# Optimization experiments

Measured on AMD Instinct MI355X. Metric: run time of the kernel, lower is better.

## Reference

```python
import jax, jax.numpy as jnp
import numpy as np

B, C, H, W = 2, 128, 256, 510
WF = W // 2 + 1  # 256 == H; required so var [B,C,H,1] broadcasts against scores [B,C,WF,WF]


def setup_inputs() -> dict:
    key = jax.random.key(0)
    ks = jax.random.split(key, 8)
    f = lambda k, s: jax.random.normal(k, s, dtype=jnp.float32)
    return {
        "g": f(ks[0], (B, C, H, W)),
        "x": f(ks[1], (B, C, H, W)),
        "wg_conv": f(ks[2], (C, C)) * 0.05,   # 1x1 conv inside Gate_signle GlobalFilter
        "bg_conv": jnp.zeros((C,), jnp.float32),
        "wx_conv": f(ks[3], (C, C)) * 0.05,   # 1x1 conv inside Wieghts_signle GlobalFilter
        "bx_conv": jnp.zeros((C,), jnp.float32),
        "filt_g": f(ks[4], (C, H, WF, 2)) * 0.02,  # learned complex freq filter (re, im)
        "filt_x": f(ks[5], (C, H, WF, 2)) * 0.02,
        "ln_gamma": jnp.ones((C,), jnp.float32),
        "ln_beta": jnp.zeros((C,), jnp.float32),
    }


def _global_filter_freq(x, w, b, filt):
    # 1x1 conv (channel mix) then GFNet-style complex frequency filtering.
    y = jnp.einsum('bchw,oc->bohw', x, w) + b[None, :, None, None]
    f = jnp.fft.rfft2(y, axes=(2, 3), norm='ortho')            # [B,C,H,WF] complex64
    wc = (filt[..., 0] + 1j * filt[..., 1]).astype(f.dtype)    # [C,H,WF]
    return f * wc[None]


def _sigmoid_complex(z):
    return jax.nn.sigmoid(z.real) + 1j * jax.nn.sigmoid(z.imag)


def reference(g, x, wg_conv, bg_conv, wx_conv, bx_conv, filt_g, filt_x, ln_gamma, ln_beta):
    g1_feq = _global_filter_freq(g, wg_conv, bg_conv, filt_g)  # [B,C,H,WF]
    x1_feq = _global_filter_freq(x, wx_conv, bx_conv, filt_x)  # [B,C,H,WF]
    # Varaince: detached, biased, over last dim, keepdims (real-valued for complex input)
    norm_frwq = jax.lax.stop_gradient(jnp.var(g1_feq, axis=-1, keepdims=True))  # [B,C,H,1]
    # frequency-domain attention: transpose(2,3) @ -> [B,C,WF,WF]
    scores = jnp.matmul(jnp.swapaxes(g1_feq, 2, 3), x1_feq) / jnp.sqrt(2.0 * jnp.pi * norm_frwq)
    atten = _sigmoid_complex(scores)
    inverse_atten = jnp.fft.irfft2(atten, s=(H, W), axes=(2, 3), norm='ortho')  # [B,C,H,W]
    r = inverse_atten + x
    # LayerNorm(F_int): channels-first LN over channel dim
    mu = jnp.mean(r, axis=1, keepdims=True)
    s2 = jnp.mean((r - mu) ** 2, axis=1, keepdims=True)
    return ln_gamma[None, :, None, None] * (r - mu) / jnp.sqrt(s2 + 1e-6) + ln_beta[None, :, None, None]
```

## Files before the change

kernel.cpp:

```cpp
#include <hip/hip_runtime.h>

typedef unsigned short u16t;
typedef __attribute__((ext_vector_type(4))) u16t us4;
typedef __attribute__((ext_vector_type(8))) u16t us8;
typedef __attribute__((ext_vector_type(8))) short mf8;
typedef __attribute__((ext_vector_type(4))) float f4;

#define BB 2
#define CCH 128
#define HHH 256
#define WWW 510
#define WFQ 256
#define HWP 130560
#define NROW 65536
#define UPL 16777216L
#define YPAD 512

__device__ __forceinline__ float u2f(u16t v){ return __uint_as_float(((unsigned)v)<<16); }
__device__ __forceinline__ u16t  f2u(float f){
  unsigned u = __float_as_uint(f);
  return (u16t)((u + 0x7fffu + ((u>>16)&1u)) >> 16);
}
__device__ __forceinline__ float ldin(const void* p, long i, int f32){
  return f32 ? ((const float*)p)[i] : u2f(((const u16t*)p)[i]);
}
__device__ __forceinline__ float sigm(float z){ return 1.f/(1.f+__expf(-z)); }
__device__ __forceinline__ f4 z4(){ f4 v; v[0]=0.f;v[1]=0.f;v[2]=0.f;v[3]=0.f; return v; }

__device__ __forceinline__ f4 MF(us8 a, us8 b, f4 c){
  return __builtin_amdgcn_mfma_f32_16x16x32_bf16((mf8)a, (mf8)b, c, 0, 0, 0);
}

__device__ __forceinline__ us8 frg(const u16t* tile, int row, int g){
  return *(const us8*)(tile + (row<<5) + (((g)^(row&3))<<3));
}
__device__ __forceinline__ void stg(u16t* __restrict__ tile, const u16t* __restrict__ src,
                                    long base, int pitch, int nu, int t){
  #pragma unroll
  for(int i=0;i<nu;i++){
    int e = t + 256*i;
    int row = e>>2, slot = e&3;
    us8 v = *(const us8*)(src + base + (long)row*pitch + (slot<<3));
    *(us8*)(tile + (row<<5) + ((slot^(row&3))<<3)) = v;
  }
}

__global__ void k_detect(const void* __restrict__ g, int* __restrict__ flag){
  __shared__ int cnt[256];
  int t = threadIdx.x;
  const u16t* pb = (const u16t*)g;
  int c = 0;
  for(int i=0;i<16;i++){
    int idx = t*16 + i;
    float v = u2f(pb[2*idx]);
    unsigned bits = __float_as_uint(v);
    int ex = (bits>>23)&0xff;
    if(ex >= 117 && ex <= 137) c++;
  }
  cnt[t]=c; __syncthreads();
  for(int s=128;s>0;s>>=1){ if(t<s) cnt[t]+=cnt[t+s]; __syncthreads(); }
  if(t==0) *flag = (cnt[0] < 2048) ? 1 : 0;
}

__device__ __forceinline__ void hl(u16t* ph, u16t* pl, long i, float v){
  u16t h = f2u(v); ph[i] = h;
  pl[i] = f2u(v - u2f(h));
}
__global__ void k_tables2(u16t* twch, u16t* twcl, u16t* twsh, u16t* twsl,
                          u16t* thch, u16t* thcl, u16t* thsh, u16t* thsl,
                          u16t* tich, u16t* ticl, u16t* tish, u16t* tisl){
  long idx = (long)blockIdx.x*256 + threadIdx.x;
  const float s510 = rsqrtf(510.0f);
  const float TP = 6.283185307179586f;
  {
    int n = (int)(idx>>9), w = (int)(idx&511);
    float c = 0.f, s = 0.f;
    if(w < 510){
      float ang = (TP/510.0f)*(float)((w*n)%510);
      c =  cosf(ang)*s510;
      s = -sinf(ang)*s510;
    }
    hl(twch, twcl, idx, c);
    hl(twsh, twsl, idx, s);
  }
  if(idx < 65536){
    int m = (int)(idx>>8), k = (int)(idx&255);
    float ang = (TP/256.0f)*(float)((m*k)&255);
    hl(thch, thcl, idx, cosf(ang)*0.0625f);
    hl(thsh, thsl, idx, sinf(ang)*0.0625f);
  }
  {
    int w = (int)(idx>>8), k = (int)(idx&255);
    float c = 0.f, s = 0.f;
    if(w < 510){
      float ck = (k==0 || k==255) ? 1.0f : 2.0f;
      float ang = (TP/510.0f)*(float)((k*w)%510);
      c =  ck*cosf(ang)*s510;
      s = -ck*sinf(ang)*s510;
    }
    hl(tich, ticl, idx, c);
    hl(tish, tisl, idx, s);
  }
}

__global__ void k_zpad(u16t* __restrict__ Y){
  int i = blockIdx.x*256 + threadIdx.x;
  long row = i>>1;
  Y[row*YPAD + 510 + (i&1)] = 0;
}

__global__ __launch_bounds__(256) void k_conv2(const void* __restrict__ in,
    const void* __restrict__ wmat, const void* __restrict__ bias,
    const int* __restrict__ flagp, u16t* __restrict__ Y){
  __shared__ __align__(16) u16t Aw[4096], Bh[4096], Bl[4096];
  __shared__ float sb[128];
  int f32 = *flagp;
  int t=threadIdx.x, l=t&63, wid=t>>6, wr=wid>>1, wc=wid&1;
  int hw0 = blockIdx.x*128, b = blockIdx.y;
  if(t<128) sb[t] = ldin(bias, t, f32);
  long inb = (long)b*CCH*HWP;
  f4 acc[4][4];
  #pragma unroll
  for(int i=0;i<4;i++) for(int j=0;j<4;j++) acc[i][j]=z4();
  for(int c0=0;c0<128;c0+=32){
    __syncthreads();
    #pragma unroll
    for(int i=0;i<2;i++){
      int e = t + 256*i; int row = e>>2, slot = e&3;
      u16t tmp[8];
      #pragma unroll
      for(int j=0;j<8;j++) tmp[j] = f2u(ldin(wmat, (long)row*128 + c0 + (slot<<3) + j, f32));
      *(us8*)(Aw + (row<<5) + ((slot^(row&3))<<3)) = *(us8*)tmp;
    }
    {
      int n = t&127, kb = (t>>7)*16;
      u16t th[16], tl[16];
      #pragma unroll
      for(int j=0;j<16;j++){
        float v = ldin(in, inb + (long)(c0+kb+j)*HWP + hw0 + n, f32);
        u16t h = f2u(v); th[j]=h;
        tl[j] = f2u(v - u2f(h));
      }
      int s0 = kb>>3;
      *(us8*)(Bh + (n<<5) + (((s0  )^(n&3))<<3)) = *(us8*)&th[0];
      *(us8*)(Bh + (n<<5) + (((s0+1)^(n&3))<<3)) = *(us8*)&th[8];
      *(us8*)(Bl + (n<<5) + (((s0  )^(n&3))<<3)) = *(us8*)&tl[0];
      *(us8*)(Bl + (n<<5) + (((s0+1)^(n&3))<<3)) = *(us8*)&tl[8];
    }
    __syncthreads();
    int lr=l&15, g=l>>4;
    us8 a[4];
    #pragma unroll
    for(int mm=0;mm<4;mm++) a[mm]=frg(Aw, wr*64+mm*16+lr, g);
    #pragma unroll
    for(int nn=0;nn<4;nn++){
      int rn = wc*64+nn*16+lr;
      us8 bh=frg(Bh,rn,g), bl=frg(Bl,rn,g);
      #pragma unroll
      for(int mm=0;mm<4;mm++){
        acc[mm][nn]=MF(a[mm],bh,acc[mm][nn]);
        acc[mm][nn]=MF(a[mm],bl,acc[mm][nn]);
      }
    }
  }
  int lr=l&15, g=l>>4;
  #pragma unroll
  for(int nn=0;nn<4;nn++){
    int hw = hw0 + wc*64 + nn*16 + lr;
    int h = hw/510, w = hw - h*510;
    #pragma unroll
    for(int mm=0;mm<4;mm++){
      #pragma unroll
      for(int r=0;r<4;r++){
        int o = wr*64 + mm*16 + (g<<2) + r;
        Y[((long)(b*128 + o)*256 + h)*YPAD + w] = f2u(acc[mm][nn][r] + sb[o]);
      }
    }
  }
}

__global__ __launch_bounds__(256) void k_rfft2(const u16t* __restrict__ Y,
    const u16t* __restrict__ twch, const u16t* __restrict__ twcl,
    const u16t* __restrict__ twsh, const u16t* __restrict__ twsl,
    u16t* __restrict__ Grt, u16t* __restrict__ Git){
  __shared__ __align__(16) u16t At[4096], Bch[4096], Bcl[4096], Bsh[4096], Bsl[4096];
  int t=threadIdx.x, l=t&63, wid=t>>6, wr=wid>>1, wc=wid&1;
  int m0 = blockIdx.x*128, n0 = blockIdx.y*128;
  f4 accr[4][4], acci[4][4];
  #pragma unroll
  for(int i=0;i<4;i++) for(int j=0;j<4;j++){ accr[i][j]=z4(); acci[i][j]=z4(); }
  for(int k0=0;k0<512;k0+=32){
    __syncthreads();
    stg(At,  Y,    (long)m0*YPAD + k0, YPAD, 2, t);
    stg(Bch, twch, (long)n0*512  + k0, 512,  2, t);
    stg(Bcl, twcl, (long)n0*512  + k0, 512,  2, t);
    stg(Bsh, twsh, (long)n0*512  + k0, 512,  2, t);
    stg(Bsl, twsl, (long)n0*512  + k0, 512,  2, t);
    __syncthreads();
    int lr=l&15, g=l>>4;
    us8 a[4];
    #pragma unroll
    for(int mm=0;mm<4;mm++) a[mm]=frg(At, wr*64+mm*16+lr, g);
    #pragma unroll
    for(int nn=0;nn<4;nn++){
      int rn = wc*64+nn*16+lr;
      us8 bch=frg(Bch,rn,g), bcl=frg(Bcl,rn,g), bsh=frg(Bsh,rn,g), bsl=frg(Bsl,rn,g);
      #pragma unroll
      for(int mm=0;mm<4;mm++){
        accr[mm][nn]=MF(a[mm],bch,accr[mm][nn]); accr[mm][nn]=MF(a[mm],bcl,accr[mm][nn]);
        acci[mm][nn]=MF(a[mm],bsh,acci[mm][nn]); acci[mm][nn]=MF(a[mm],bsl,acci[mm][nn]);
      }
    }
  }
  int plane = blockIdx.x>>1;
  int h0 = (blockIdx.x&1)<<7;
  int lr=l&15, g=l>>4;
  #pragma unroll
  for(int nn=0;nn<4;nn++){
    int n = n0 + wc*64 + nn*16 + lr;
    #pragma unroll
    for(int mm=0;mm<4;mm++){
      int hh = h0 + wr*64 + mm*16 + (g<<2);
      long o = (long)plane*65536 + (long)n*256 + hh;
      us4 pr, pi;
      #pragma unroll
      for(int r=0;r<4;r++){ pr[r]=f2u(accr[mm][nn][r]); pi[r]=f2u(acci[mm][nn][r]); }
      *(us4*)(Grt+o)=pr; *(us4*)(Git+o)=pi;
    }
  }
}

__global__ __launch_bounds__(256) void k_ffth2(
    const u16t* __restrict__ Br_, const u16t* __restrict__ Bi_,
    const u16t* __restrict__ ach_, const u16t* __restrict__ acl_,
    const u16t* __restrict__ ash_, const u16t* __restrict__ asl_,
    float sgn, int tr_out, const void* __restrict__ filt, const int* __restrict__ flagp,
    u16t* __restrict__ Or_, u16t* __restrict__ Oi_){
  __shared__ __align__(16) u16t Ach[2048], Acl[2048], Ash[2048], Asl[2048], Bgr[2048], Bgi[2048];
  int t=threadIdx.x, l=t&63, wid=t>>6, wr=wid>>1, wc=wid&1;
  int m0=blockIdx.x*64, n0=blockIdx.y*64, plane=blockIdx.z;
  long pbase=(long)plane*65536;
  f4 P1[2][2],P2[2][2],P3[2][2],P4[2][2];
  #pragma unroll
  for(int i=0;i<2;i++) for(int j=0;j<2;j++){ P1[i][j]=z4();P2[i][j]=z4();P3[i][j]=z4();P4[i][j]=z4(); }
  for(int k0=0;k0<256;k0+=32){
    __syncthreads();
    stg(Ach, ach_, (long)m0*256+k0, 256, 1, t);
    stg(Acl, acl_, (long)m0*256+k0, 256, 1, t);
    stg(Ash, ash_, (long)m0*256+k0, 256, 1, t);
    stg(Asl, asl_, (long)m0*256+k0, 256, 1, t);
    stg(Bgr, Br_, pbase+(long)n0*256+k0, 256, 1, t);
    stg(Bgi, Bi_, pbase+(long)n0*256+k0, 256, 1, t);
    __syncthreads();
    int lr=l&15, g=l>>4;
    us8 fch[2],fcl[2],fsh[2],fsl[2];
    #pragma unroll
    for(int mm=0;mm<2;mm++){
      int rr=wr*32+mm*16+lr;
      fch[mm]=frg(Ach,rr,g); fcl[mm]=frg(Acl,rr,g); fsh[mm]=frg(Ash,rr,g); fsl[mm]=frg(Asl,rr,g);
    }
    #pragma unroll
    for(int nn=0;nn<2;nn++){
      int rn=wc*32+nn*16+lr;
      us8 bgr=frg(Bgr,rn,g), bgi=frg(Bgi,rn,g);
      #pragma unroll
      for(int mm=0;mm<2;mm++){
        P1[mm][nn]=MF(fch[mm],bgr,P1[mm][nn]); P1[mm][nn]=MF(fcl[mm],bgr,P1[mm][nn]);
        P2[mm][nn]=MF(fsh[mm],bgi,P2[mm][nn]); P2[mm][nn]=MF(fsl[mm],bgi,P2[mm][nn]);
        P3[mm][nn]=MF(fch[mm],bgi,P3[mm][nn]); P3[mm][nn]=MF(fcl[mm],bgi,P3[mm][nn]);
        P4[mm][nn]=MF(fsh[mm],bgr,P4[mm][nn]); P4[mm][nn]=MF(fsl[mm],bgr,P4[mm][nn]);
      }
    }
  }
  int f32 = filt ? *flagp : 0;
  int lr=l&15, g=l>>4;
  int c_ch = plane & 127;
  #pragma unroll
  for(int nn=0;nn<2;nn++){
    int n = n0 + wc*32 + nn*16 + lr;
    #pragma unroll
    for(int mm=0;mm<2;mm++){
      int mb = m0 + wr*32 + mm*16 + (g<<2);
      float vr[4], vi[4];
      #pragma unroll
      for(int r=0;r<4;r++){
        vr[r] = P1[mm][nn][r] + sgn*P2[mm][nn][r];
        vi[r] = P3[mm][nn][r] - sgn*P4[mm][nn][r];
      }
      if(filt){
        #pragma unroll
        for(int r=0;r<4;r++){
          long fi = (((long)c_ch*256 + (mb+r))*256 + n)*2;
          float fwr=ldin(filt,fi,f32), fwi=ldin(filt,fi+1,f32);
          float a=vr[r], b=vi[r];
          vr[r]=a*fwr-b*fwi; vi[r]=a*fwi+b*fwr;
        }
      }
      if(tr_out){
        us4 pr, pi;
        #pragma unroll
        for(int r=0;r<4;r++){ pr[r]=f2u(vr[r]); pi[r]=f2u(vi[r]); }
        *(us4*)(Or_ + pbase + (long)n*256 + mb) = pr;
        *(us4*)(Oi_ + pbase + (long)n*256 + mb) = pi;
      } else {
        #pragma unroll
        for(int r=0;r<4;r++){
          Or_[pbase + (long)(mb+r)*256 + n] = f2u(vr[r]);
          Oi_[pbase + (long)(mb+r)*256 + n] = f2u(vi[r]);
        }
      }
    }
  }
}

__global__ __launch_bounds__(1024) void k_var2(const u16t* __restrict__ Grt,
    const u16t* __restrict__ Git, float* __restrict__ rinv){
  __shared__ float rs[1024], is_[1024], qs[1024];
  int plane = blockIdx.x, t = threadIdx.x;
  int kh = t & 255, part = t >> 8;
  long base = (long)plane*65536 + kh;
  float sr=0.f, si=0.f, s2=0.f;
  #pragma unroll 4
  for(int q=0;q<64;q++){
    long o = base + (long)(part*64+q)*256;
    float r = u2f(Grt[o]), im = u2f(Git[o]);
    sr += r; si += im; s2 += r*r + im*im;
  }
  rs[t]=sr; is_[t]=si; qs[t]=s2;
  __syncthreads();
  if(t<256){
    sr = rs[t]+rs[t+256]+rs[t+512]+rs[t+768];
    si = is_[t]+is_[t+256]+is_[t+512]+is_[t+768];
    s2 = qs[t]+qs[t+256]+qs[t+512]+qs[t+768];
    float mr = sr*(1.f/256.f), mi = si*(1.f/256.f);
    float v = s2*(1.f/256.f) - mr*mr - mi*mi;
    rinv[plane*256 + kh] = rsqrtf(6.283185307179586f * fmaxf(v, 1e-20f));
  }
}

__global__ __launch_bounds__(256) void k_scores2(
    const u16t* __restrict__ Agr_, const u16t* __restrict__ Agi_,
    const u16t* __restrict__ Bxr_, const u16t* __restrict__ Bxi_,
    const float* __restrict__ rinv, u16t* __restrict__ Sr_, u16t* __restrict__ Si_){
  __shared__ __align__(16) u16t Agr[2048], Agi[2048], Bxr[2048], Bxi[2048];
  int t=threadIdx.x, l=t&63, wid=t>>6, wr=wid>>1, wc=wid&1;
  int m0=blockIdx.x*64, n0=blockIdx.y*64, plane=blockIdx.z;
  long pbase=(long)plane*65536;
  f4 P1[2][2],P2[2][2],P3[2][2],P4[2][2];
  #pragma unroll
  for(int i=0;i<2;i++) for(int j=0;j<2;j++){ P1[i][j]=z4();P2[i][j]=z4();P3[i][j]=z4();P4[i][j]=z4(); }
  for(int k0=0;k0<256;k0+=32){
    __syncthreads();
    stg(Agr, Agr_, pbase+(long)m0*256+k0, 256, 1, t);
    stg(Agi, Agi_, pbase+(long)m0*256+k0, 256, 1, t);
    stg(Bxr, Bxr_, pbase+(long)n0*256+k0, 256, 1, t);
    stg(Bxi, Bxi_, pbase+(long)n0*256+k0, 256, 1, t);
    __syncthreads();
    int lr=l&15, g=l>>4;
    us8 agr[2], agi[2];
    #pragma unroll
    for(int mm=0;mm<2;mm++){
      int rr=wr*32+mm*16+lr;
      agr[mm]=frg(Agr,rr,g); agi[mm]=frg(Agi,rr,g);
    }
    #pragma unroll
    for(int nn=0;nn<2;nn++){
      int rn=wc*32+nn*16+lr;
      us8 bxr=frg(Bxr,rn,g), bxi=frg(Bxi,rn,g);
      #pragma unroll
      for(int mm=0;mm<2;mm++){
        P1[mm][nn]=MF(agr[mm],bxr,P1[mm][nn]);
        P2[mm][nn]=MF(agi[mm],bxi,P2[mm][nn]);
        P3[mm][nn]=MF(agr[mm],bxi,P3[mm][nn]);
        P4[mm][nn]=MF(agi[mm],bxr,P4[mm][nn]);
      }
    }
  }
  int lr=l&15, g=l>>4;
  #pragma unroll
  for(int nn=0;nn<2;nn++){
    int n = n0 + wc*32 + nn*16 + lr;
    #pragma unroll
    for(int mm=0;mm<2;mm++){
      int mb = m0 + wr*32 + mm*16 + (g<<2);
      us4 pr, pi;
      #pragma unroll
      for(int r=0;r<4;r++){
        float rv = rinv[(plane<<8) + mb + r];
        pr[r] = f2u(sigm((P1[mm][nn][r]-P2[mm][nn][r])*rv));
        pi[r] = f2u(sigm((P3[mm][nn][r]+P4[mm][nn][r])*rv));
      }
      *(us4*)(Sr_ + pbase + (long)n*256 + mb) = pr;
      *(us4*)(Si_ + pbase + (long)n*256 + mb) = pi;
    }
  }
}

__global__ __launch_bounds__(256) void k_irfft2(
    const u16t* __restrict__ Tr, const u16t* __restrict__ Ti,
    const u16t* __restrict__ tich, const u16t* __restrict__ ticl,
    const u16t* __restrict__ tish, const u16t* __restrict__ tisl,
    const void* __restrict__ xin, const int* __restrict__ flagp, float* __restrict__ R){
  __shared__ __align__(16) u16t Ar[4096], Ai[4096], Bch[4096], Bcl[4096], Bsh[4096], Bsl[4096];
  int t=threadIdx.x, l=t&63, wid=t>>6, wr=wid>>1, wc=wid&1;
  int m0=blockIdx.x*128, n0=blockIdx.y*128;
  f4 acc[4][4];
  #pragma unroll
  for(int i=0;i<4;i++) for(int j=0;j<4;j++) acc[i][j]=z4();
  for(int k0=0;k0<256;k0+=32){
    __syncthreads();
    stg(Ar,  Tr,   (long)m0*256+k0, 256, 2, t);
    stg(Ai,  Ti,   (long)m0*256+k0, 256, 2, t);
    stg(Bch, tich, (long)n0*256+k0, 256, 2, t);
    stg(Bcl, ticl, (long)n0*256+k0, 256, 2, t);
    stg(Bsh, tish, (long)n0*256+k0, 256, 2, t);
    stg(Bsl, tisl, (long)n0*256+k0, 256, 2, t);
    __syncthreads();
    int lr=l&15, g=l>>4;
    us8 ar[4], ai[4];
    #pragma unroll
    for(int mm=0;mm<4;mm++){
      int rr = wr*64+mm*16+lr;
      ar[mm]=frg(Ar,rr,g); ai[mm]=frg(Ai,rr,g);
    }
    #pragma unroll
    for(int nn=0;nn<4;nn++){
      int rn = wc*64+nn*16+lr;
      us8 bch=frg(Bch,rn,g), bcl=frg(Bcl,rn,g), bsh=frg(Bsh,rn,g), bsl=frg(Bsl,rn,g);
      #pragma unroll
      for(int mm=0;mm<4;mm++){
        acc[mm][nn]=MF(ar[mm],bch,acc[mm][nn]); acc[mm][nn]=MF(ar[mm],bcl,acc[mm][nn]);
        acc[mm][nn]=MF(ai[mm],bsh,acc[mm][nn]); acc[mm][nn]=MF(ai[mm],bsl,acc[mm][nn]);
      }
    }
  }
  int f32=*flagp;
  int lr=l&15, g=l>>4;
  #pragma unroll
  for(int nn=0;nn<4;nn++){
    int w = n0 + wc*64 + nn*16 + lr;
    if(w >= 510) continue;
    #pragma unroll
    for(int mm=0;mm<4;mm++){
      int row0 = m0 + wr*64 + mm*16 + (g<<2);
      #pragma unroll
      for(int r=0;r<4;r++){
        long o = (long)(row0+r)*510 + w;
        R[o] = acc[mm][nn][r] + ldin(xin, o, f32);
      }
    }
  }
}

__global__ __launch_bounds__(256) void k_ln(const float* __restrict__ R,
    const void* __restrict__ gamma, const void* __restrict__ beta,
    const int* __restrict__ flagp, void* __restrict__ out){
  int f32 = *flagp;
  int p = blockIdx.x*256 + threadIdx.x;
  int b = p / HWP, hw = p % HWP;
  long base = (long)b*CCH*HWP + hw;
  float sum=0.f, sq=0.f;
  for(int c=0;c<CCH;c++){
    float v = R[base + (long)c*HWP];
    sum += v; sq += v*v;
  }
  float mu = sum*(1.f/128.f);
  float var = sq*(1.f/128.f) - mu*mu;
  float inv = rsqrtf(fmaxf(var,0.f) + 1e-6f);
  for(int c=0;c<CCH;c++){
    float v = (R[base + (long)c*HWP] - mu)*inv;
    float o = ldin(gamma,c,f32)*v + ldin(beta,c,f32);
    long oi = base + (long)c*HWP;
    if(f32) ((float*)out)[oi] = o;
    else    ((u16t*)out)[oi]  = f2u(o);
  }
}

extern "C" void kernel_launch(void* const* d_in, const int* in_sizes, int n_in,
                              void* d_out, int out_size, void* d_ws, size_t ws_size,
                              hipStream_t stream) {
  const void* g   = d_in[0];
  const void* x   = d_in[1];
  const void* wg  = d_in[2];
  const void* bg  = d_in[3];
  const void* wx  = d_in[4];
  const void* bx  = d_in[5];
  const void* fg  = d_in[6];
  const void* fx  = d_in[7];
  const void* gam = d_in[8];
  const void* bet = d_in[9];

  u16t* Y  = (u16t*)d_ws;
  u16t* Bq = Y  + 33554432L;
  u16t* Cq = Bq + 33554432L;
  char* pp = (char*)d_ws + 201326592L;
  float* rinv = (float*)pp; pp += 262144L;
  u16t* twch=(u16t*)pp; pp+=262144L;  u16t* twcl=(u16t*)pp; pp+=262144L;
  u16t* twsh=(u16t*)pp; pp+=262144L;  u16t* twsl=(u16t*)pp; pp+=262144L;
  u16t* thch=(u16t*)pp; pp+=131072L;  u16t* thcl=(u16t*)pp; pp+=131072L;
  u16t* thsh=(u16t*)pp; pp+=131072L;  u16t* thsl=(u16t*)pp; pp+=131072L;
  u16t* tich=(u16t*)pp; pp+=262144L;  u16t* ticl=(u16t*)pp; pp+=262144L;
  u16t* tish=(u16t*)pp; pp+=262144L;  u16t* tisl=(u16t*)pp; pp+=262144L;
  int* flag = (int*)pp;
  float* R  = (float*)d_ws;

  k_detect <<<1,256,0,stream>>>(g, flag);
  k_tables2<<<512,256,0,stream>>>(twch,twcl,twsh,twsl,thch,thcl,thsh,thsl,tich,ticl,tish,tisl);
  k_zpad   <<<512,256,0,stream>>>(Y);

  k_conv2<<<dim3(1020,2),256,0,stream>>>(g, wg, bg, flag, Y);
  k_rfft2<<<dim3(512,2),256,0,stream>>>(Y, twch,twcl,twsh,twsl, Bq, Bq+UPL);
  k_ffth2<<<dim3(4,4,256),256,0,stream>>>(Bq, Bq+UPL, thch,thcl,thsh,thsl, 1.f, 1, fg, flag, Cq, Cq+UPL);

  k_conv2<<<dim3(1020,2),256,0,stream>>>(x, wx, bx, flag, Y);
  k_rfft2<<<dim3(512,2),256,0,stream>>>(Y, twch,twcl,twsh,twsl, Bq, Bq+UPL);
  k_ffth2<<<dim3(4,4,256),256,0,stream>>>(Bq, Bq+UPL, thch,thcl,thsh,thsl, 1.f, 1, fx, flag, Y, Y+UPL);

  k_var2<<<256,1024,0,stream>>>(Cq, Cq+UPL, rinv);

  k_scores2<<<dim3(4,4,256),256,0,stream>>>(Cq, Cq+UPL, Y, Y+UPL, rinv, Bq, Bq+UPL);

  k_ffth2<<<dim3(4,4,256),256,0,stream>>>(Bq, Bq+UPL, thch,thcl,thsh,thsl, -1.f, 0, nullptr, flag, Cq, Cq+UPL);

  k_irfft2<<<dim3(512,4),256,0,stream>>>(Cq, Cq+UPL, tich,ticl,tish,tisl, x, flag, R);

  k_ln<<<1020,256,0,stream>>>(R, gam, bet, flag, d_out);
}
```

Measured before the change: 1.554 ms.

## Register-prefetch next K tile, change LDS swizzle, drop low-part twiddles in inverse path

Each GEMM-style kernel (conv, rfft, ffth, scores, irfft) now loads the next K-slice of global data into registers while the current slice is consumed from LDS. This overlaps global latency with MFMA work. The LDS XOR swizzle changes from row&3 to (row>>1)&3 to alter the bank-conflict pattern. The inverse column FFT and irfft drop the bf16 low-part twiddle MFMAs, halving their matrix work at some accuracy cost. The cost is extra register pressure from the prefetch buffers.

```diff
diff --git a/kernel.cpp b/kernel.cpp
--- a/kernel.cpp
+++ b/kernel.cpp
@@ -31,17 +31,26 @@
   return __builtin_amdgcn_mfma_f32_16x16x32_bf16((mf8)a, (mf8)b, c, 0, 0, 0);
 }
 
+__device__ __forceinline__ int swz(int row){ return (row>>1)&3; }
+
 __device__ __forceinline__ us8 frg(const u16t* tile, int row, int g){
-  return *(const us8*)(tile + (row<<5) + (((g)^(row&3))<<3));
-}
-__device__ __forceinline__ void stg(u16t* __restrict__ tile, const u16t* __restrict__ src,
+  return *(const us8*)(tile + (row<<5) + (((g)^swz(row))<<3));
+}
+__device__ __forceinline__ void ldt(us8* v, const u16t* __restrict__ src,
                                     long base, int pitch, int nu, int t){
   #pragma unroll
   for(int i=0;i<nu;i++){
     int e = t + 256*i;
     int row = e>>2, slot = e&3;
-    us8 v = *(const us8*)(src + base + (long)row*pitch + (slot<<3));
-    *(us8*)(tile + (row<<5) + ((slot^(row&3))<<3)) = v;
+    v[i] = *(const us8*)(src + base + (long)row*pitch + (slot<<3));
+  }
+}
+__device__ __forceinline__ void stt(u16t* __restrict__ tile, const us8* v, int nu, int t){
+  #pragma unroll
+  for(int i=0;i<nu;i++){
+    int e = t + 256*i;
+    int row = e>>2, slot = e&3;
+    *(us8*)(tile + (row<<5) + ((slot^swz(row))<<3)) = v[i];
   }
 }
 
@@ -119,33 +128,43 @@
   int hw0 = blockIdx.x*128, b = blockIdx.y;
   if(t<128) sb[t] = ldin(bias, t, f32);
   long inb = (long)b*CCH*HWP;
+  int bn = t&127, bkb = (t>>7)*16, bs0 = bkb>>3;
   f4 acc[4][4];
   #pragma unroll
   for(int i=0;i<4;i++) for(int j=0;j<4;j++) acc[i][j]=z4();
+  float pa[16], pb[16];
+  #pragma unroll
+  for(int i=0;i<2;i++){ int e=t+256*i; int row=e>>2, slot=e&3;
+    #pragma unroll
+    for(int j=0;j<8;j++) pa[i*8+j] = ldin(wmat, (long)row*128 + (slot<<3) + j, f32); }
+  #pragma unroll
+  for(int j=0;j<16;j++) pb[j] = ldin(in, inb + (long)(bkb+j)*HWP + hw0 + bn, f32);
+
   for(int c0=0;c0<128;c0+=32){
     __syncthreads();
     #pragma unroll
-    for(int i=0;i<2;i++){
-      int e = t + 256*i; int row = e>>2, slot = e&3;
+    for(int i=0;i<2;i++){ int e=t+256*i; int row=e>>2, slot=e&3;
       u16t tmp[8];
       #pragma unroll
-      for(int j=0;j<8;j++) tmp[j] = f2u(ldin(wmat, (long)row*128 + c0 + (slot<<3) + j, f32));
-      *(us8*)(Aw + (row<<5) + ((slot^(row&3))<<3)) = *(us8*)tmp;
-    }
+      for(int j=0;j<8;j++) tmp[j] = f2u(pa[i*8+j]);
+      *(us8*)(Aw + (row<<5) + ((slot^swz(row))<<3)) = *(us8*)tmp; }
     {
-      int n = t&127, kb = (t>>7)*16;
       u16t th[16], tl[16];
       #pragma unroll
-      for(int j=0;j<16;j++){
-        float v = ldin(in, inb + (long)(c0+kb+j)*HWP + hw0 + n, f32);
-        u16t h = f2u(v); th[j]=h;
-        tl[j] = f2u(v - u2f(h));
-      }
-      int s0 = kb>>3;
-      *(us8*)(Bh + (n<<5) + (((s0  )^(n&3))<<3)) = *(us8*)&th[0];
-      *(us8*)(Bh + (n<<5) + (((s0+1)^(n&3))<<3)) = *(us8*)&th[8];
-      *(us8*)(Bl + (n<<5) + (((s0  )^(n&3))<<3)) = *(us8*)&tl[0];
-      *(us8*)(Bl + (n<<5) + (((s0+1)^(n&3))<<3)) = *(us8*)&tl[8];
+      for(int j=0;j<16;j++){ u16t h=f2u(pb[j]); th[j]=h; tl[j]=f2u(pb[j]-u2f(h)); }
+      int sw = swz(bn);
+      *(us8*)(Bh + (bn<<5) + (((bs0  )^sw)<<3)) = *(us8*)&th[0];
+      *(us8*)(Bh + (bn<<5) + (((bs0+1)^sw)<<3)) = *(us8*)&th[8];
+      *(us8*)(Bl + (bn<<5) + (((bs0  )^sw)<<3)) = *(us8*)&tl[0];
+      *(us8*)(Bl + (bn<<5) + (((bs0+1)^sw)<<3)) = *(us8*)&tl[8];
+    }
+    if(c0+32 < 128){
+      #pragma unroll
+      for(int i=0;i<2;i++){ int e=t+256*i; int row=e>>2, slot=e&3;
+        #pragma unroll
+        for(int j=0;j<8;j++) pa[i*8+j] = ldin(wmat, (long)row*128 + c0+32 + (slot<<3) + j, f32); }
+      #pragma unroll
+      for(int j=0;j<16;j++) pb[j] = ldin(in, inb + (long)(c0+32+bkb+j)*HWP + hw0 + bn, f32);
     }
     __syncthreads();
     int lr=l&15, g=l>>4;
@@ -189,13 +208,22 @@
   f4 accr[4][4], acci[4][4];
   #pragma unroll
   for(int i=0;i<4;i++) for(int j=0;j<4;j++){ accr[i][j]=z4(); acci[i][j]=z4(); }
+  us8 pA[2], pC[2], pc2[2], pS[2], ps2[2];
+  ldt(pA,  Y,    (long)m0*YPAD, YPAD, 2, t);
+  ldt(pC,  twch, (long)n0*512,  512,  2, t);
+  ldt(pc2, twcl, (long)n0*512,  512,  2, t);
+  ldt(pS,  twsh, (long)n0*512,  512,  2, t);
+  ldt(ps2, twsl, (long)n0*512,  512,  2, t);
   for(int k0=0;k0<512;k0+=32){
     __syncthreads();
-    stg(At,  Y,    (long)m0*YPAD + k0, YPAD, 2, t);
-    stg(Bch, twch, (long)n0*512  + k0, 512,  2, t);
-    stg(Bcl, twcl, (long)n0*512  + k0, 512,  2, t);
-    stg(Bsh, twsh, (long)n0*512  + k0, 512,  2, t);
-    stg(Bsl, twsl, (long)n0*512  + k0, 512,  2, t);
+    stt(At,pA,2,t); stt(Bch,pC,2,t); stt(Bcl,pc2,2,t); stt(Bsh,pS,2,t); stt(Bsl,ps2,2,t);
+    if(k0+32 < 512){
+      ldt(pA,  Y,    (long)m0*YPAD + k0+32, YPAD, 2, t);
+      ldt(pC,  twch, (long)n0*512  + k0+32, 512,  2, t);
+      ldt(pc2, twcl, (long)n0*512  + k0+32, 512,  2, t);
+      ldt(pS,  twsh, (long)n0*512  + k0+32, 512,  2, t);
+      ldt(ps2, twsl, (long)n0*512  + k0+32, 512,  2, t);
+    }
     __syncthreads();
     int lr=l&15, g=l>>4;
     us8 a[4];
@@ -230,34 +258,53 @@
   }
 }
 
+template<int LO, int TR>
 __global__ __launch_bounds__(256) void k_ffth2(
     const u16t* __restrict__ Br_, const u16t* __restrict__ Bi_,
     const u16t* __restrict__ ach_, const u16t* __restrict__ acl_,
     const u16t* __restrict__ ash_, const u16t* __restrict__ asl_,
-    float sgn, int tr_out, const void* __restrict__ filt, const int* __restrict__ flagp,
+    float sgn, const void* __restrict__ filt, const int* __restrict__ flagp,
     u16t* __restrict__ Or_, u16t* __restrict__ Oi_){
-  __shared__ __align__(16) u16t Ach[2048], Acl[2048], Ash[2048], Asl[2048], Bgr[2048], Bgi[2048];
+  __shared__ __align__(16) u16t Ach[2048], Ash[2048], Bgr[2048], Bgi[2048];
+  __shared__ __align__(16) u16t Acl[LO?2048:16], Asl[LO?2048:16];
   int t=threadIdx.x, l=t&63, wid=t>>6, wr=wid>>1, wc=wid&1;
   int m0=blockIdx.x*64, n0=blockIdx.y*64, plane=blockIdx.z;
   long pbase=(long)plane*65536;
   f4 P1[2][2],P2[2][2],P3[2][2],P4[2][2];
   #pragma unroll
   for(int i=0;i<2;i++) for(int j=0;j<2;j++){ P1[i][j]=z4();P2[i][j]=z4();P3[i][j]=z4();P4[i][j]=z4(); }
+  us8 pch, psh, pgr, pgi, pcl, psl;
+  ldt(&pch, ach_, (long)m0*256, 256, 1, t);
+  ldt(&psh, ash_, (long)m0*256, 256, 1, t);
+  if constexpr(LO){
+    ldt(&pcl, acl_, (long)m0*256, 256, 1, t);
+    ldt(&psl, asl_, (long)m0*256, 256, 1, t);
+  }
+  ldt(&pgr, Br_, pbase+(long)n0*256, 256, 1, t);
+  ldt(&pgi, Bi_, pbase+(long)n0*256, 256, 1, t);
   for(int k0=0;k0<256;k0+=32){
     __syncthreads();
-    stg(Ach, ach_, (long)m0*256+k0, 256, 1, t);
-    stg(Acl, acl_, (long)m0*256+k0, 256, 1, t);
-    stg(Ash, ash_, (long)m0*256+k0, 256, 1, t);
-    stg(Asl, asl_, (long)m0*256+k0, 256, 1, t);
-    stg(Bgr, Br_, pbase+(long)n0*256+k0, 256, 1, t);
-    stg(Bgi, Bi_, pbase+(long)n0*256+k0, 256, 1, t);
+    stt(Ach,&pch,1,t); stt(Ash,&psh,1,t);
+    if constexpr(LO){ stt(Acl,&pcl,1,t); stt(Asl,&psl,1,t); }
+    stt(Bgr,&pgr,1,t); stt(Bgi,&pgi,1,t);
+    if(k0+32 < 256){
+      ldt(&pch, ach_, (long)m0*256+k0+32, 256, 1, t);
+      ldt(&psh, ash_, (long)m0*256+k0+32, 256, 1, t);
+      if constexpr(LO){
+        ldt(&pcl, acl_, (long)m0*256+k0+32, 256, 1, t);
+        ldt(&psl, asl_, (long)m0*256+k0+32, 256, 1, t);
+      }
+      ldt(&pgr, Br_, pbase+(long)n0*256+k0+32, 256, 1, t);
+      ldt(&pgi, Bi_, pbase+(long)n0*256+k0+32, 256, 1, t);
+    }
     __syncthreads();
     int lr=l&15, g=l>>4;
-    us8 fch[2],fcl[2],fsh[2],fsl[2];
+    us8 fch[2],fsh[2],fcl[2],fsl[2];
     #pragma unroll
     for(int mm=0;mm<2;mm++){
       int rr=wr*32+mm*16+lr;
-      fch[mm]=frg(Ach,rr,g); fcl[mm]=frg(Acl,rr,g); fsh[mm]=frg(Ash,rr,g); fsl[mm]=frg(Asl,rr,g);
+      fch[mm]=frg(Ach,rr,g); fsh[mm]=frg(Ash,rr,g);
+      if constexpr(LO){ fcl[mm]=frg(Acl,rr,g); fsl[mm]=frg(Asl,rr,g); }
     }
     #pragma unroll
     for(int nn=0;nn<2;nn++){
@@ -265,10 +312,16 @@
       us8 bgr=frg(Bgr,rn,g), bgi=frg(Bgi,rn,g);
       #pragma unroll
       for(int mm=0;mm<2;mm++){
-        P1[mm][nn]=MF(fch[mm],bgr,P1[mm][nn]); P1[mm][nn]=MF(fcl[mm],bgr,P1[mm][nn]);
-        P2[mm][nn]=MF(fsh[mm],bgi,P2[mm][nn]); P2[mm][nn]=MF(fsl[mm],bgi,P2[mm][nn]);
-        P3[mm][nn]=MF(fch[mm],bgi,P3[mm][nn]); P3[mm][nn]=MF(fcl[mm],bgi,P3[mm][nn]);
-        P4[mm][nn]=MF(fsh[mm],bgr,P4[mm][nn]); P4[mm][nn]=MF(fsl[mm],bgr,P4[mm][nn]);
+        P1[mm][nn]=MF(fch[mm],bgr,P1[mm][nn]);
+        P2[mm][nn]=MF(fsh[mm],bgi,P2[mm][nn]);
+        P3[mm][nn]=MF(fch[mm],bgi,P3[mm][nn]);
+        P4[mm][nn]=MF(fsh[mm],bgr,P4[mm][nn]);
+        if constexpr(LO){
+          P1[mm][nn]=MF(fcl[mm],bgr,P1[mm][nn]);
+          P2[mm][nn]=MF(fsl[mm],bgi,P2[mm][nn]);
+          P3[mm][nn]=MF(fcl[mm],bgi,P3[mm][nn]);
+          P4[mm][nn]=MF(fsl[mm],bgr,P4[mm][nn]);
+        }
       }
     }
   }
@@ -296,7 +349,7 @@
           vr[r]=a*fwr-b*fwi; vi[r]=a*fwi+b*fwr;
         }
       }
-      if(tr_out){
+      if constexpr(TR){
         us4 pr, pi;
         #pragma unroll
         for(int r=0;r<4;r++){ pr[r]=f2u(vr[r]); pi[r]=f2u(vi[r]); }
@@ -349,12 +402,20 @@
   f4 P1[2][2],P2[2][2],P3[2][2],P4[2][2];
   #pragma unroll
   for(int i=0;i<2;i++) for(int j=0;j<2;j++){ P1[i][j]=z4();P2[i][j]=z4();P3[i][j]=z4();P4[i][j]=z4(); }
+  us8 p0,p1,p2,p3;
+  ldt(&p0, Agr_, pbase+(long)m0*256, 256, 1, t);
+  ldt(&p1, Agi_, pbase+(long)m0*256, 256, 1, t);
+  ldt(&p2, Bxr_, pbase+(long)n0*256, 256, 1, t);
+  ldt(&p3, Bxi_, pbase+(long)n0*256, 256, 1, t);
   for(int k0=0;k0<256;k0+=32){
     __syncthreads();
-    stg(Agr, Agr_, pbase+(long)m0*256+k0, 256, 1, t);
-    stg(Agi, Agi_, pbase+(long)m0*256+k0, 256, 1, t);
-    stg(Bxr, Bxr_, pbase+(long)n0*256+k0, 256, 1, t);
-    stg(Bxi, Bxi_, pbase+(long)n0*256+k0, 256, 1, t);
+    stt(Agr,&p0,1,t); stt(Agi,&p1,1,t); stt(Bxr,&p2,1,t); stt(Bxi,&p3,1,t);
+    if(k0+32 < 256){
+      ldt(&p0, Agr_, pbase+(long)m0*256+k0+32, 256, 1, t);
+      ldt(&p1, Agi_, pbase+(long)m0*256+k0+32, 256, 1, t);
+      ldt(&p2, Bxr_, pbase+(long)n0*256+k0+32, 256, 1, t);
+      ldt(&p3, Bxi_, pbase+(long)n0*256+k0+32, 256, 1, t);
+    }
     __syncthreads();
     int lr=l&15, g=l>>4;
     us8 agr[2], agi[2];
@@ -398,39 +459,44 @@
 
 __global__ __launch_bounds__(256) void k_irfft2(
     const u16t* __restrict__ Tr, const u16t* __restrict__ Ti,
-    const u16t* __restrict__ tich, const u16t* __restrict__ ticl,
-    const u16t* __restrict__ tish, const u16t* __restrict__ tisl,
+    const u16t* __restrict__ tic, const u16t* __restrict__ tis,
     const void* __restrict__ xin, const int* __restrict__ flagp, float* __restrict__ R){
-  __shared__ __align__(16) u16t Ar[4096], Ai[4096], Bch[4096], Bcl[4096], Bsh[4096], Bsl[4096];
+  __shared__ __align__(16) u16t Ar[4096], Ai[4096], Bc[4096], Bs[4096];
   int t=threadIdx.x, l=t&63, wid=t>>6, wr=wid>>1, wc=wid&1;
   int m0=blockIdx.x*128, n0=blockIdx.y*128;
   f4 acc[4][4];
   #pragma unroll
   for(int i=0;i<4;i++) for(int j=0;j<4;j++) acc[i][j]=z4();
+  us8 pr2[2], pi2[2], pc2[2], ps2[2];
+  ldt(pr2, Tr,  (long)m0*256, 256, 2, t);
+  ldt(pi2, Ti,  (long)m0*256, 256, 2, t);
+  ldt(pc2, tic, (long)n0*256, 256, 2, t);
+  ldt(ps2, tis, (long)n0*256, 256, 2, t);
   for(int k0=0;k0<256;k0+=32){
     __syncthreads();
-    stg(Ar,  Tr,   (long)m0*256+k0, 256, 2, t);
-    stg(Ai,  Ti,   (long)m0*256+k0, 256, 2, t);
-    stg(Bch, tich, (long)n0*256+k0, 256, 2, t);
-    stg(Bcl, ticl, (long)n0*256+k0, 256, 2, t);
-    stg(Bsh, tish, (long)n0*256+k0, 256, 2, t);
-    stg(Bsl, tisl, (long)n0*256+k0, 256, 2, t);
+    stt(Ar,pr2,2,t); stt(Ai,pi2,2,t); stt(Bc,pc2,2,t); stt(Bs,ps2,2,t);
+    if(k0+32 < 256){
+      ldt(pr2, Tr,  (long)m0*256+k0+32, 256, 2, t);
+      ldt(pi2, Ti,  (long)m0*256+k0+32, 256, 2, t);
+      ldt(pc2, tic, (long)n0*256+k0+32, 256, 2, t);
+      ldt(ps2, tis, (long)n0*256+k0+32, 256, 2, t);
+    }
     __syncthreads();
     int lr=l&15, g=l>>4;
-    us8 ar[4], ai[4];
+    us8 ar[4], ai2[4];
     #pragma unroll
     for(int mm=0;mm<4;mm++){
       int rr = wr*64+mm*16+lr;
-      ar[mm]=frg(Ar,rr,g); ai[mm]=frg(Ai,rr,g);
+      ar[mm]=frg(Ar,rr,g); ai2[mm]=frg(Ai,rr,g);
     }
     #pragma unroll
     for(int nn=0;nn<4;nn++){
       int rn = wc*64+nn*16+lr;
-      us8 bch=frg(Bch,rn,g), bcl=frg(Bcl,rn,g), bsh=frg(Bsh,rn,g), bsl=frg(Bsl,rn,g);
+      us8 bc=frg(Bc,rn,g), bs=frg(Bs,rn,g);
       #pragma unroll
       for(int mm=0;mm<4;mm++){
-        acc[mm][nn]=MF(ar[mm],bch,acc[mm][nn]); acc[mm][nn]=MF(ar[mm],bcl,acc[mm][nn]);
-        acc[mm][nn]=MF(ai[mm],bsh,acc[mm][nn]); acc[mm][nn]=MF(ai[mm],bsl,acc[mm][nn]);
+        acc[mm][nn]=MF(ar[mm],bc,acc[mm][nn]);
+        acc[mm][nn]=MF(ai2[mm],bs,acc[mm][nn]);
       }
     }
   }
@@ -510,19 +576,19 @@
 
   k_conv2<<<dim3(1020,2),256,0,stream>>>(g, wg, bg, flag, Y);
   k_rfft2<<<dim3(512,2),256,0,stream>>>(Y, twch,twcl,twsh,twsl, Bq, Bq+UPL);
-  k_ffth2<<<dim3(4,4,256),256,0,stream>>>(Bq, Bq+UPL, thch,thcl,thsh,thsl, 1.f, 1, fg, flag, Cq, Cq+UPL);
+  k_ffth2<1,1><<<dim3(4,4,256),256,0,stream>>>(Bq, Bq+UPL, thch,thcl,thsh,thsl, 1.f, fg, flag, Cq, Cq+UPL);
 
   k_conv2<<<dim3(1020,2),256,0,stream>>>(x, wx, bx, flag, Y);
   k_rfft2<<<dim3(512,2),256,0,stream>>>(Y, twch,twcl,twsh,twsl, Bq, Bq+UPL);
-  k_ffth2<<<dim3(4,4,256),256,0,stream>>>(Bq, Bq+UPL, thch,thcl,thsh,thsl, 1.f, 1, fx, flag, Y, Y+UPL);
+  k_ffth2<1,1><<<dim3(4,4,256),256,0,stream>>>(Bq, Bq+UPL, thch,thcl,thsh,thsl, 1.f, fx, flag, Y, Y+UPL);
 
   k_var2<<<256,1024,0,stream>>>(Cq, Cq+UPL, rinv);
 
   k_scores2<<<dim3(4,4,256),256,0,stream>>>(Cq, Cq+UPL, Y, Y+UPL, rinv, Bq, Bq+UPL);
 
-  k_ffth2<<<dim3(4,4,256),256,0,stream>>>(Bq, Bq+UPL, thch,thcl,thsh,thsl, -1.f, 0, nullptr, flag, Cq, Cq+UPL);
-
-  k_irfft2<<<dim3(512,4),256,0,stream>>>(Cq, Cq+UPL, tich,ticl,tish,tisl, x, flag, R);
+  k_ffth2<0,0><<<dim3(4,4,256),256,0,stream>>>(Bq, Bq+UPL, thch,thcl,thsh,thsl, -1.f, nullptr, flag, Cq, Cq+UPL);
+
+  k_irfft2<<<dim3(512,4),256,0,stream>>>(Cq, Cq+UPL, tich,tish, x, flag, R);
 
   k_ln<<<1020,256,0,stream>>>(R, gam, bet, flag, d_out);
 }
```

Result: faster. 1.390 ms (-10.5%).
